# Kernel optimization log

Hardware: AMD Instinct MI355X
Metric: run time of the kernel (lower is better)

The kernel has to match this reference:

```python
import jax, jax.numpy as jnp
import numpy as np

N = 100000
E = 1600000
NODE_DIM = 64
H = 128
NUM_LAYERS = 3
NUM_CLASSES = 6
NUM_GRAPHS = 512
LN_EPS = 1e-5


def setup_inputs() -> dict:
    key = jax.random.key(0)
    ks = jax.random.split(key, 16)
    s = 0.05
    x = jax.random.normal(ks[0], (N, NODE_DIM), jnp.float32)
    edge_index = jax.random.randint(ks[1], (2, E), 0, N, dtype=jnp.int64)
    batch = jnp.sort(jax.random.randint(ks[2], (N,), 0, NUM_GRAPHS, dtype=jnp.int64))
    return {
        "x": x,
        "edge_index": edge_index,
        "batch": batch,
        "proj_w": jax.random.normal(ks[3], (NODE_DIM, H), jnp.float32) * s,
        "proj_b": jnp.zeros((H,), jnp.float32),
        "lin_l_w": jax.random.normal(ks[4], (NUM_LAYERS, H, H), jnp.float32) * s,
        "lin_l_b": jnp.zeros((NUM_LAYERS, H), jnp.float32),
        "lin_r_w": jax.random.normal(ks[5], (NUM_LAYERS, H, H), jnp.float32) * s,
        "ln_g": jnp.ones((NUM_LAYERS, H), jnp.float32),
        "ln_b": jnp.zeros((NUM_LAYERS, H), jnp.float32),
        "gate_w1": jax.random.normal(ks[6], (H, H // 2), jnp.float32) * s,
        "gate_b1": jnp.zeros((H // 2,), jnp.float32),
        "gate_w2": jax.random.normal(ks[7], (H // 2, 1), jnp.float32) * s,
        "gate_b2": jnp.zeros((1,), jnp.float32),
        "cls_w1": jax.random.normal(ks[8], (H, H // 2), jnp.float32) * s,
        "cls_b1": jnp.zeros((H // 2,), jnp.float32),
        "cls_w2": jax.random.normal(ks[9], (H // 2, NUM_CLASSES), jnp.float32) * s,
        "cls_b2": jnp.zeros((NUM_CLASSES,), jnp.float32),
    }


def _layer_norm(x, g, b):
    mu = jnp.mean(x, axis=-1, keepdims=True)
    var = jnp.mean(jnp.square(x - mu), axis=-1, keepdims=True)
    return (x - mu) * jax.lax.rsqrt(var + LN_EPS) * g + b


def _sage_mean_aggr(x, src, dst):
    # mean of source node features grouped by destination node
    summed = jax.ops.segment_sum(x[src], dst, num_segments=N)  # [N,H]
    deg = jax.ops.segment_sum(jnp.ones((E,), x.dtype), dst, num_segments=N)
    return summed / jnp.maximum(deg, 1.0)[:, None]


def reference(x, edge_index, batch, proj_w, proj_b, lin_l_w, lin_l_b, lin_r_w,
              ln_g, ln_b, gate_w1, gate_b1, gate_w2, gate_b2,
              cls_w1, cls_b1, cls_w2, cls_b2):
    src, dst = edge_index[0], edge_index[1]
    h = jax.nn.relu(x @ proj_w + proj_b)  # [N,H]
    for l in range(NUM_LAYERS):
        r = h
        aggr = _sage_mean_aggr(h, src, dst)
        # PyG SAGEConv: lin_l(aggregated) + lin_r(self), bias only in lin_l
        h = aggr @ lin_l_w[l] + lin_l_b[l] + h @ lin_r_w[l]
        h = _layer_norm(h, ln_g[l], ln_b[l])
        h = jax.nn.elu(h)
        h = h + r  # dropout is identity in eval mode
    # GlobalAttention pooling: segment softmax over nodes per graph
    gate = (jax.nn.relu(h @ gate_w1 + gate_b1) @ gate_w2 + gate_b2)[:, 0]  # [N]
    gmax = jax.ops.segment_max(gate, batch, num_segments=NUM_GRAPHS)
    eg = jnp.exp(gate - gmax[batch])
    denom = jax.ops.segment_sum(eg, batch, num_segments=NUM_GRAPHS)
    alpha = eg / denom[batch]  # [N]
    pooled = jax.ops.segment_sum(h * alpha[:, None], batch, num_segments=NUM_GRAPHS)  # [G,H]
    out = jax.nn.relu(pooled @ cls_w1 + cls_b1) @ cls_w2 + cls_b2  # [G,C]
    return out
```

## Files before the change

### kernel.cpp

```cpp
#include <hip/hip_runtime.h>
#include <hip/hip_fp16.h>
#include <math.h>

#define N_NODES   100000
#define N_EDGES   1600000
#define NDIM      64
#define H         128
#define NUM_LAYERS 3
#define NUM_CLASSES 6
#define NUM_GRAPHS 512
#define LN_EPS    1e-5f
#define NBKT      391
#define SCAP      5376
#define BPAD      136

typedef _Float16 f16x8 __attribute__((ext_vector_type(8)));
typedef float    f32x4 __attribute__((ext_vector_type(4)));

__device__ __forceinline__ int idx_at(const int* raw, int is64, int i) {
    return is64 ? raw[2 * (long long)i] : raw[i];
}
__device__ __forceinline__ int lower_bound(const int* a, int n, int v) {
    int lo = 0, hi = n;
    while (lo < hi) { int m = (lo + hi) >> 1; if (a[m] < v) lo = m + 1; else hi = m; }
    return lo;
}

__device__ __forceinline__ f32x4 gload16(const __half* __restrict__ base, int voff) {
    f32x4 r;
    asm volatile("global_load_dwordx4 %0, %1, %2"
                 : "=v"(r) : "v"(voff), "s"(base));
    return r;
}

__global__ void k_detect(const int* eraw, const int* braw, int* flags,
                         int* bcnt, float* gate_z) {
    int i = blockIdx.x * blockDim.x + threadIdx.x;
    if (i < 512) bcnt[i] = 0;
    if (i < 64) gate_z[i] = 0.f;
    if (i == 0) {
        int e64 = 1;
        for (int k = 1; k < 128; k += 2) if (eraw[k] != 0) { e64 = 0; break; }
        flags[0] = e64;
        flags[1] = (braw[N_NODES - 1] == 0) ? 1 : 0;
    }
}

__global__ void k_conv_batch(const int* braw, const int* flags, int* batch32) {
    int i = blockIdx.x * blockDim.x + threadIdx.x;
    if (i < N_NODES) batch32[i] = idx_at(braw, flags[1], i);
}

__global__ __launch_bounds__(256) void k_bhist(const int* eraw, const int* flags, int* bcnt) {
    __shared__ int c[512];
    int tid = threadIdx.x;
    for (int i = tid; i < 512; i += 256) c[i] = 0;
    __syncthreads();
    int f = flags[0];
    int stride = gridDim.x * 256;
    for (int e = blockIdx.x * 256 + tid; e < N_EDGES; e += stride) {
        int d = idx_at(eraw, f, N_EDGES + e);
        atomicAdd(&c[d >> 8], 1);
    }
    __syncthreads();
    for (int i = tid; i < 512; i += 256) if (c[i]) atomicAdd(&bcnt[i], c[i]);
}

__global__ void k_bscan(const int* bcnt, int* boff, int* bcursor) {
    __shared__ int sh[512];
    int tid = threadIdx.x;
    int v = bcnt[tid];
    sh[tid] = v;
    __syncthreads();
    for (int off = 1; off < 512; off <<= 1) {
        int u = (tid >= off) ? sh[tid - off] : 0;
        __syncthreads();
        sh[tid] += u;
        __syncthreads();
    }
    int excl = sh[tid] - v;
    boff[tid] = excl;
    bcursor[tid] = excl;
    if (tid == 511) boff[512] = sh[511];
}

#define EPB 4096
__global__ __launch_bounds__(256) void k_bucket(const int* eraw, const int* flags,
                                                int* bcursor, unsigned int* br) {
    __shared__ int cnt[512];
    __shared__ int excl[512];
    __shared__ int resv[512];
    __shared__ int lcur[512];
    __shared__ int psum[256];
    __shared__ unsigned int srec[EPB];
    __shared__ unsigned short sbkt[EPB];
    int tid = threadIdx.x;
    int f = flags[0];
    int base = blockIdx.x * EPB;
    int se[16], de[16];
#pragma unroll
    for (int j = 0; j < 16; ++j) {
        int e = base + j * 256 + tid;
        if (e < N_EDGES) {
            se[j] = idx_at(eraw, f, e);
            de[j] = idx_at(eraw, f, N_EDGES + e);
        } else de[j] = -1;
    }
    for (int i = tid; i < 512; i += 256) cnt[i] = 0;
    __syncthreads();
#pragma unroll
    for (int j = 0; j < 16; ++j)
        if (de[j] >= 0) atomicAdd(&cnt[de[j] >> 8], 1);
    __syncthreads();
    int b0 = cnt[2 * tid], b1 = cnt[2 * tid + 1];
    psum[tid] = b0 + b1;
    __syncthreads();
    for (int off = 1; off < 256; off <<= 1) {
        int u = (tid >= off) ? psum[tid - off] : 0;
        __syncthreads();
        psum[tid] += u;
        __syncthreads();
    }
    int pex = psum[tid] - (b0 + b1);
    excl[2 * tid] = pex;
    excl[2 * tid + 1] = pex + b0;
    lcur[2 * tid] = pex;
    lcur[2 * tid + 1] = pex + b0;
    resv[2 * tid]     = b0 ? atomicAdd(&bcursor[2 * tid], b0) : 0;
    resv[2 * tid + 1] = b1 ? atomicAdd(&bcursor[2 * tid + 1], b1) : 0;
    __syncthreads();
#pragma unroll
    for (int j = 0; j < 16; ++j)
        if (de[j] >= 0) {
            int b = de[j] >> 8;
            int slot = atomicAdd(&lcur[b], 1);
            srec[slot] = ((unsigned int)(de[j] & 255) << 24) | (unsigned int)se[j];
            sbkt[slot] = (unsigned short)b;
        }
    __syncthreads();
    int vtot = psum[255];
    for (int s2 = tid; s2 < vtot; s2 += 256) {
        int b = sbkt[s2];
        br[resv[b] + (s2 - excl[b])] = srec[s2];
    }
}

__global__ __launch_bounds__(256) void k_csr_tail(const unsigned int* br, const int* boff,
                                                  int* rowptr, int* col) {
    __shared__ int d256[256];
    __shared__ int sc[256];
    __shared__ int cbuf[SCAP];
    int b = blockIdx.x;
    int tid = threadIdx.x;
    int lo = boff[b], hi = boff[b + 1];
    int wsize = hi - lo;
    d256[tid] = 0;
    __syncthreads();
    for (int i = lo + tid; i < hi; i += 256)
        atomicAdd(&d256[br[i] >> 24], 1);
    __syncthreads();
    int v = d256[tid];
    sc[tid] = v;
    __syncthreads();
    for (int off = 1; off < 256; off <<= 1) {
        int u = (tid >= off) ? sc[tid - off] : 0;
        __syncthreads();
        sc[tid] += u;
        __syncthreads();
    }
    int excl = sc[tid] - v;
    int node = (b << 8) + tid;
    if (node < N_NODES) rowptr[node] = lo + excl;
    if (b == NBKT - 1 && tid == 0) rowptr[N_NODES] = N_EDGES;
    __syncthreads();
    d256[tid] = excl;
    __syncthreads();
    if (wsize <= SCAP) {
        for (int i = lo + tid; i < hi; i += 256) {
            unsigned int r = br[i];
            int p = atomicAdd(&d256[r >> 24], 1);
            cbuf[p] = (int)(r & 0xFFFFFF);
        }
        __syncthreads();
        for (int j = tid; j < wsize; j += 256) col[lo + j] = cbuf[j] << 8;
    } else {
        for (int i = lo + tid; i < hi; i += 256) {
            unsigned int r = br[i];
            int p = atomicAdd(&d256[r >> 24], 1);
            col[lo + p] = (int)(r & 0xFFFFFF) << 8;
        }
    }
}

__global__ void k_prepw(const float* __restrict__ lin_l_w, const float* __restrict__ lin_r_w,
                        const float* __restrict__ gate_w1,
                        __half* __restrict__ W16t, __half* __restrict__ W16g) {
    int i = blockIdx.x * 256 + threadIdx.x;
    if (i < NUM_LAYERS * 128 * 256) {
        int l = i >> 15;
        int rem = i & 32767;
        int n = rem >> 8;
        int k = rem & 255;
        float v = (k < 128) ? lin_l_w[(size_t)l * 16384 + k * 128 + n]
                            : lin_r_w[(size_t)l * 16384 + (k - 128) * 128 + n];
        W16t[(size_t)l * 32768 + n * 256 + k] = __float2half(v);
    } else if (i < NUM_LAYERS * 128 * 256 + 64 * 128) {
        int idx = i - NUM_LAYERS * 128 * 256;
        int n = idx >> 7;
        int k = idx & 127;
        W16g[n * 128 + k] = __float2half(gate_w1[k * 64 + n]);
    }
}

__global__ __launch_bounds__(256) void k_gemm_proj(const float* __restrict__ A,
                                                   const float* __restrict__ W,
                                                   const float* __restrict__ bias,
                                                   __half* __restrict__ C16,
                                                   int nrows, int K) {
    __shared__ float As_t[32][68];
    __shared__ float Ws[32 * 128];
    int tid = threadIdx.x;
    int row0 = blockIdx.x * 64;
    int tr = tid >> 4;
    int tc = tid & 15;
    int c0 = tc * 8;
    float acc[4][8];
#pragma unroll
    for (int i = 0; i < 4; ++i)
#pragma unroll
        for (int j = 0; j < 8; ++j) acc[i][j] = 0.f;

    for (int kc = 0; kc < K; kc += 32) {
        __syncthreads();
#pragma unroll
        for (int it = 0; it < 2; ++it) {
            int idx = tid + it * 256;
            int r = idx >> 3, c4 = idx & 7;
            int gr = row0 + r;
            float4 v = make_float4(0.f, 0.f, 0.f, 0.f);
            if (gr < nrows) v = *(const float4*)(A + (size_t)gr * K + kc + c4 * 4);
            As_t[c4 * 4 + 0][r] = v.x;
            As_t[c4 * 4 + 1][r] = v.y;
            As_t[c4 * 4 + 2][r] = v.z;
            As_t[c4 * 4 + 3][r] = v.w;
        }
#pragma unroll
        for (int it = 0; it < 4; ++it) {
            int idx = tid + it * 256;
            int r = idx >> 5, c4 = idx & 31;
            *(float4*)(&Ws[r * 128 + c4 * 4]) = *(const float4*)(W + (size_t)(kc + r) * 128 + c4 * 4);
        }
        __syncthreads();
#pragma unroll
        for (int k = 0; k < 32; ++k) {
            float4 a4 = *(const float4*)(&As_t[k][tr * 4]);
            float a[4] = {a4.x, a4.y, a4.z, a4.w};
            float4 w0 = *(const float4*)(&Ws[k * 128 + c0]);
            float4 w1 = *(const float4*)(&Ws[k * 128 + c0 + 4]);
            float w[8] = {w0.x, w0.y, w0.z, w0.w, w1.x, w1.y, w1.z, w1.w};
#pragma unroll
            for (int i = 0; i < 4; ++i)
#pragma unroll
                for (int j = 0; j < 8; ++j) acc[i][j] += a[i] * w[j];
        }
    }
    float bv[8];
#pragma unroll
    for (int j = 0; j < 8; ++j) bv[j] = bias[c0 + j];
#pragma unroll
    for (int i = 0; i < 4; ++i) {
        int gr = row0 + tr * 4 + i;
        if (gr < nrows) {
            float o[8];
#pragma unroll
            for (int j = 0; j < 8; ++j) o[j] = fmaxf(acc[i][j] + bv[j], 0.f);
            __half2 p[4];
#pragma unroll
            for (int j = 0; j < 8; j += 2) p[j / 2] = __floats2half2_rn(o[j], o[j + 1]);
            *(float4*)(C16 + (size_t)gr * 128 + c0) = *(float4*)p;
        }
    }
}

__global__ __launch_bounds__(256) void k_gate_mfma(const __half* __restrict__ h16,
                                                   const __half* __restrict__ W16g,
                                                   const float* __restrict__ b1,
                                                   const float* __restrict__ w2,
                                                   const float* __restrict__ b2,
                                                   float* __restrict__ gate) {
    __shared__ __half Bs[64 * BPAD];
    int tid = threadIdx.x;
    int wave = tid >> 6, lane = tid & 63;
    int s = lane & 15, quad = lane >> 4;
    int row0 = blockIdx.x * 64 + wave * 16;
    int arow = row0 + s;
    if (arow >= N_NODES) arow = N_NODES - 1;

#pragma unroll
    for (int it = 0; it < 4; ++it) {
        int idx = tid + it * 256;
        int n = idx >> 4, ch = idx & 15;
        *(float4*)(&Bs[n * BPAD + ch * 8]) = *(const float4*)(W16g + (size_t)n * 128 + ch * 8);
    }
    __syncthreads();

    f32x4 acc[4];
#pragma unroll
    for (int c = 0; c < 4; ++c) acc[c] = (f32x4){0.f, 0.f, 0.f, 0.f};

    const __half* aptr = h16 + (size_t)arow * H;
#pragma unroll
    for (int kc = 0; kc < 128; kc += 32) {
        f16x8 afrag = *(const f16x8*)(aptr + kc + quad * 8);
#pragma unroll
        for (int c = 0; c < 4; ++c) {
            f16x8 bfrag = *(const f16x8*)(&Bs[(c * 16 + s) * BPAD + kc + quad * 8]);
            acc[c] = __builtin_amdgcn_mfma_f32_16x16x32_f16(afrag, bfrag, acc[c], 0, 0, 0);
        }
    }
    float part[4] = {0.f, 0.f, 0.f, 0.f};
#pragma unroll
    for (int c = 0; c < 4; ++c) {
        float bv = b1[c * 16 + s];
        float wv = w2[c * 16 + s];
#pragma unroll
        for (int i = 0; i < 4; ++i)
            part[i] += fmaxf(acc[c][i] + bv, 0.f) * wv;
    }
#pragma unroll
    for (int off = 1; off < 16; off <<= 1) {
#pragma unroll
        for (int i = 0; i < 4; ++i) part[i] += __shfl_xor(part[i], off);
    }
    if (s == 0) {
        float b2v = b2[0];
#pragma unroll
        for (int i = 0; i < 4; ++i) {
            int r = row0 + quad * 4 + i;
            if (r < N_NODES) gate[r] = part[i] + b2v;
        }
    }
}

__global__ __launch_bounds__(64) void k_softmax_g(float* __restrict__ gate,
                                                  const int* __restrict__ batch32,
                                                  float* __restrict__ gsum) {
    int g = blockIdx.x;
    int lane = threadIdx.x;
    int n0 = lower_bound(batch32, N_NODES, g);
    int n1 = lower_bound(batch32, N_NODES, g + 1);
    float m = -INFINITY;
    for (int n = n0 + lane; n < n1; n += 64) m = fmaxf(m, gate[n]);
#pragma unroll
    for (int off = 32; off >= 1; off >>= 1) m = fmaxf(m, __shfl_xor(m, off));
    float s = 0.f;
    for (int n = n0 + lane; n < n1; n += 64) {
        float e = expf(gate[n] - m);
        gate[n] = e;
        s += e;
    }
#pragma unroll
    for (int off = 32; off >= 1; off >>= 1) s += __shfl_xor(s, off);
    if (lane == 0) gsum[g] = s;
}

__global__ __launch_bounds__(256) void k_pool_g(const __half* __restrict__ h16,
                                                const float* __restrict__ eg,
                                                const float* __restrict__ gsum,
                                                const int* __restrict__ batch32,
                                                float* __restrict__ pooled) {
    __shared__ float sx[256], sy[256];
    int g = blockIdx.x;
    int tid = threadIdx.x;
    int c2 = tid & 63;
    int p = tid >> 6;
    int n0 = lower_bound(batch32, N_NODES, g);
    int n1 = lower_bound(batch32, N_NODES, g + 1);
    float ax = 0.f, ay = 0.f;
    for (int n = n0 + p; n < n1; n += 4) {
        __half2 v = *(const __half2*)(h16 + (size_t)n * H + c2 * 2);
        float2 fv = __half22float2(v);
        float w = eg[n];
        ax += w * fv.x;
        ay += w * fv.y;
    }
    sx[tid] = ax; sy[tid] = ay;
    __syncthreads();
    if (tid < 64) {
        float s = gsum[g];
        float vx = sx[tid] + sx[tid + 64] + sx[tid + 128] + sx[tid + 192];
        float vy = sy[tid] + sy[tid + 64] + sy[tid + 128] + sy[tid + 192];
        float2 o;
        o.x = (n1 > n0) ? vx / s : 0.f;
        o.y = (n1 > n0) ? vy / s : 0.f;
        *(float2*)(pooled + (size_t)g * H + c2 * 2) = o;
    }
}

__global__ __launch_bounds__(256) void k_layer_mfma(const __half* __restrict__ t16,
                                                    __half* __restrict__ h16,
                                                    const __half* __restrict__ W16t,
                                                    const float* __restrict__ bl,
                                                    const float* __restrict__ g,
                                                    const float* __restrict__ bb) {
    __shared__ __half Bs[128 * BPAD];
    int tid = threadIdx.x;
    int wave = tid >> 6, lane = tid & 63;
    int s = lane & 15, quad = lane >> 4;
    int row0 = blockIdx.x * 64;
    int wrow0 = row0 + wave * 16;
    int arow = wrow0 + s;
    if (arow >= N_NODES) arow = N_NODES - 1;

    f32x4 acc[8];
#pragma unroll
    for (int c = 0; c < 8; ++c) acc[c] = (f32x4){0.f, 0.f, 0.f, 0.f};

#pragma unroll
    for (int ph = 0; ph < 2; ++ph) {
        __syncthreads();
#pragma unroll
        for (int it = 0; it < 8; ++it) {
            int idx = tid + it * 256;
            int n = idx >> 4, ch = idx & 15;
            *(float4*)(&Bs[n * BPAD + ch * 8]) =
                *(const float4*)(W16t + (size_t)n * 256 + ph * 128 + ch * 8);
        }
        __syncthreads();
        const __half* aptr = (ph ? h16 : t16) + (size_t)arow * H;
#pragma unroll
        for (int kk = 0; kk < 128; kk += 32) {
            f16x8 afrag = *(const f16x8*)(aptr + kk + quad * 8);
#pragma unroll
            for (int c = 0; c < 8; ++c) {
                f16x8 bfrag = *(const f16x8*)(&Bs[(c * 16 + s) * BPAD + kk + quad * 8]);
                acc[c] = __builtin_amdgcn_mfma_f32_16x16x32_f16(afrag, bfrag, acc[c], 0, 0, 0);
            }
        }
    }

    float y[8][4];
    float sm[4] = {0.f, 0.f, 0.f, 0.f}, sq[4] = {0.f, 0.f, 0.f, 0.f};
#pragma unroll
    for (int c = 0; c < 8; ++c) {
        float bv = bl[c * 16 + s];
#pragma unroll
        for (int i = 0; i < 4; ++i) {
            float v = acc[c][i] + bv;
            y[c][i] = v;
            sm[i] += v;
            sq[i] += v * v;
        }
    }
#pragma unroll
    for (int off = 1; off < 16; off <<= 1) {
#pragma unroll
        for (int i = 0; i < 4; ++i) {
            sm[i] += __shfl_xor(sm[i], off);
            sq[i] += __shfl_xor(sq[i], off);
        }
    }
    float mean[4], rstd[4];
#pragma unroll
    for (int i = 0; i < 4; ++i) {
        mean[i] = sm[i] * (1.0f / H);
        float var = sq[i] * (1.0f / H) - mean[i] * mean[i];
        rstd[i] = rsqrtf(var + LN_EPS);
    }
    float gv[8], bbv[8];
#pragma unroll
    for (int c = 0; c < 8; ++c) { gv[c] = g[c * 16 + s]; bbv[c] = bb[c * 16 + s]; }

    __syncthreads();
#pragma unroll
    for (int i = 0; i < 4; ++i) {
        int lr = wave * 16 + quad * 4 + i;
#pragma unroll
        for (int c = 0; c < 8; ++c) {
            float yv = (y[c][i] - mean[i]) * rstd[i] * gv[c] + bbv[c];
            yv = yv > 0.f ? yv : expf(yv) - 1.f;
            Bs[lr * BPAD + c * 16 + s] = __float2half(yv);
        }
    }
    __syncthreads();
#pragma unroll
    for (int it = 0; it < 4; ++it) {
        int idx = tid + it * 256;
        int r = idx >> 4, ch = idx & 15;
        int grow = row0 + r;
        if (grow < N_NODES) {
            float4 sv = *(float4*)(&Bs[r * BPAD + ch * 8]);
            float4 hv = *(const float4*)(h16 + (size_t)grow * H + ch * 8);
            __half2* pa = (__half2*)&sv;
            const __half2* pb = (const __half2*)&hv;
#pragma unroll
            for (int j = 0; j < 4; ++j) {
                float2 fa = __half22float2(pa[j]);
                float2 fb = __half22float2(pb[j]);
                pa[j] = __floats2half2_rn(fa.x + fb.x, fa.y + fb.y);
            }
            *(float4*)(h16 + (size_t)grow * H + ch * 8) = sv;
        }
    }
}

__global__ __launch_bounds__(256) void k_aggr(const __half* __restrict__ h16,
                                              const int* __restrict__ rowptr,
                                              const int* __restrict__ col,
                                              __half* __restrict__ t16,
                                              int zoff) {
    int lane = threadIdx.x & 63;
    int node = blockIdx.x * 4 + (threadIdx.x >> 6);
    if (node >= N_NODES) return;
    int s = lane & 15;
    int g = lane >> 4;
    int soff = s * 16;
    int e0 = rowptr[node];
    int deg = rowptr[node + 1] - e0;

    if (deg == 0) {
        if (g == 0) {
            float4 zz = make_float4(0.f, 0.f, 0.f, 0.f);
            *(float4*)(t16 + (size_t)node * H + s * 8) = zz;
        }
        return;
    }

    __half2 z = __floats2half2_rn(0.f, 0.f);
    __half2 ac[4][4];
#pragma unroll
    for (int a = 0; a < 4; ++a)
#pragma unroll
        for (int k = 0; k < 4; ++k) ac[a][k] = z;

    {
        int cb[8];
#pragma unroll
        for (int j = 0; j < 8; ++j) {
            int ei = g + 4 * j;
            cb[j] = col[e0 + (ei < deg ? ei : 0)];
        }
#pragma unroll
        for (int j = 0; j < 8; ++j) {
            int ei = g + 4 * j;
            cb[j] = ((ei < deg) ? cb[j] : zoff) + soff;
        }
        __builtin_amdgcn_sched_barrier(0);
        f32x4 rv[8];
#pragma unroll
        for (int j = 0; j < 8; ++j) rv[j] = gload16(h16, cb[j]);
        asm volatile("s_waitcnt vmcnt(0)" ::: "memory");
        __builtin_amdgcn_sched_barrier(0);
#pragma unroll
        for (int j = 0; j < 8; ++j) {
            const __half2* hv = (const __half2*)&rv[j];
            int a = j & 3;
            ac[a][0] = __hadd2(ac[a][0], hv[0]);
            ac[a][1] = __hadd2(ac[a][1], hv[1]);
            ac[a][2] = __hadd2(ac[a][2], hv[2]);
            ac[a][3] = __hadd2(ac[a][3], hv[3]);
        }
    }

    if (deg > 32) {
        for (int base = 32; base < deg; base += 32) {
            int cb[8];
#pragma unroll
            for (int j = 0; j < 8; ++j) {
                int ei = base + g + 4 * j;
                cb[j] = col[e0 + (ei < deg ? ei : base)];
            }
#pragma unroll
            for (int j = 0; j < 8; ++j) {
                int ei = base + g + 4 * j;
                cb[j] = ((ei < deg) ? cb[j] : zoff) + soff;
            }
            __builtin_amdgcn_sched_barrier(0);
            f32x4 rv[8];
#pragma unroll
            for (int j = 0; j < 8; ++j) rv[j] = gload16(h16, cb[j]);
            asm volatile("s_waitcnt vmcnt(0)" ::: "memory");
            __builtin_amdgcn_sched_barrier(0);
#pragma unroll
            for (int j = 0; j < 8; ++j) {
                const __half2* hv = (const __half2*)&rv[j];
                int a = j & 3;
                ac[a][0] = __hadd2(ac[a][0], hv[0]);
                ac[a][1] = __hadd2(ac[a][1], hv[1]);
                ac[a][2] = __hadd2(ac[a][2], hv[2]);
                ac[a][3] = __hadd2(ac[a][3], hv[3]);
            }
        }
    }

    float f[8];
#pragma unroll
    for (int k = 0; k < 4; ++k) {
        float2 s0 = __half22float2(ac[0][k]);
        float2 s1 = __half22float2(ac[1][k]);
        float2 s2 = __half22float2(ac[2][k]);
        float2 s3 = __half22float2(ac[3][k]);
        f[2 * k]     = (s0.x + s1.x) + (s2.x + s3.x);
        f[2 * k + 1] = (s0.y + s1.y) + (s2.y + s3.y);
    }
#pragma unroll
    for (int off = 16; off <= 32; off <<= 1) {
#pragma unroll
        for (int k = 0; k < 8; ++k) f[k] += __shfl_xor(f[k], off);
    }
    if (g == 0) {
        float inv = 1.0f / (float)(deg > 1 ? deg : 1);
        __half2 o[4];
#pragma unroll
        for (int k = 0; k < 4; ++k)
            o[k] = __floats2half2_rn(f[2 * k] * inv, f[2 * k + 1] * inv);
        *(float4*)(t16 + (size_t)node * H + s * 8) = *(float4*)o;
    }
}

__global__ __launch_bounds__(64) void k_cls(const float* __restrict__ pooled,
                                            const float* __restrict__ w1,
                                            const float* __restrict__ b1,
                                            const float* __restrict__ w2,
                                            const float* __restrict__ b2,
                                            float* __restrict__ out) {
    __shared__ float sp[64];
    int g = blockIdx.x;
    int lane = threadIdx.x;
    float r0 = pooled[(size_t)g * H + lane];
    float r1 = pooled[(size_t)g * H + 64 + lane];
    float acc = b1[lane];
#pragma unroll 16
    for (int k = 0; k < 64; ++k) acc += __shfl(r0, k) * w1[k * 64 + lane];
#pragma unroll 16
    for (int k = 0; k < 64; ++k) acc += __shfl(r1, k) * w1[(64 + k) * 64 + lane];
    sp[lane] = fmaxf(acc, 0.f);
    __syncthreads();
    if (lane < NUM_CLASSES) {
        float o = b2[lane];
        for (int c = 0; c < 64; ++c) o += sp[c] * w2[c * NUM_CLASSES + lane];
        out[g * NUM_CLASSES + lane] = o;
    }
}

extern "C" void kernel_launch(void* const* d_in, const int* in_sizes, int n_in,
                              void* d_out, int out_size, void* d_ws, size_t ws_size,
                              hipStream_t stream) {
    const float* x       = (const float*)d_in[0];
    const int*   eraw    = (const int*)d_in[1];
    const int*   braw    = (const int*)d_in[2];
    const float* proj_w  = (const float*)d_in[3];
    const float* proj_b  = (const float*)d_in[4];
    const float* lin_l_w = (const float*)d_in[5];
    const float* lin_l_b = (const float*)d_in[6];
    const float* lin_r_w = (const float*)d_in[7];
    const float* ln_g    = (const float*)d_in[8];
    const float* ln_b    = (const float*)d_in[9];
    const float* gate_w1 = (const float*)d_in[10];
    const float* gate_b1 = (const float*)d_in[11];
    const float* gate_w2 = (const float*)d_in[12];
    const float* gate_b2 = (const float*)d_in[13];
    const float* cls_w1  = (const float*)d_in[14];
    const float* cls_b1  = (const float*)d_in[15];
    const float* cls_w2  = (const float*)d_in[16];
    const float* cls_b2  = (const float*)d_in[17];
    float* out = (float*)d_out;

    __half* h16    = (__half*)d_ws;
    __half* t16    = h16 + (size_t)N_NODES * H;
    float*  gate   = (float*)(t16 + (size_t)N_NODES * H);
    float*  gsum   = gate + N_NODES;
    float*  pooled = gsum + NUM_GRAPHS;
    __half* W16t   = (__half*)(pooled + NUM_GRAPHS * H);
    __half* W16g   = W16t + (size_t)NUM_LAYERS * 32768;
    int* flags     = (int*)(W16g + 64 * 128);
    int* col       = flags + 4;
    int* batch32   = col + N_EDGES;
    int* rowptr    = batch32 + N_NODES;
    int* bcnt      = rowptr + N_NODES + 1;
    int* boff      = bcnt + 512;
    int* bcursor   = boff + 513;
    unsigned int* br = (unsigned int*)(bcursor + 512);

    const int zoff = (int)((const char*)gate - (const char*)h16);

    const int nbN = (N_NODES + 255) / 256;
    const int nbE4 = (N_EDGES + EPB - 1) / EPB;
    const int nbW = (N_NODES + 3) / 4;
    const int nbG = (N_NODES + 63) / 64;
    const int nbP = (NUM_LAYERS * 128 * 256 + 64 * 128 + 255) / 256;

    k_detect<<<2, 256, 0, stream>>>(eraw, braw, flags, bcnt, gate);
    k_conv_batch<<<nbN, 256, 0, stream>>>(braw, flags, batch32);
    k_bhist<<<512, 256, 0, stream>>>(eraw, flags, bcnt);
    k_bscan<<<1, 512, 0, stream>>>(bcnt, boff, bcursor);
    k_bucket<<<nbE4, 256, 0, stream>>>(eraw, flags, bcursor, br);
    k_csr_tail<<<NBKT, 256, 0, stream>>>(br, boff, rowptr, col);
    k_prepw<<<nbP, 256, 0, stream>>>(lin_l_w, lin_r_w, gate_w1, W16t, W16g);

    k_gemm_proj<<<nbG, 256, 0, stream>>>(x, proj_w, proj_b, h16, N_NODES, NDIM);

    for (int l = 0; l < NUM_LAYERS; ++l) {
        const float* bl  = lin_l_b + (size_t)l * H;
        const float* gl  = ln_g + (size_t)l * H;
        const float* blb = ln_b + (size_t)l * H;
        k_aggr<<<nbW, 256, 0, stream>>>(h16, rowptr, col, t16, zoff);
        k_layer_mfma<<<nbG, 256, 0, stream>>>(t16, h16, W16t + (size_t)l * 32768, bl, gl, blb);
    }

    k_gate_mfma<<<nbG, 256, 0, stream>>>(h16, W16g, gate_b1, gate_w2, gate_b2, gate);
    k_softmax_g<<<NUM_GRAPHS, 64, 0, stream>>>(gate, batch32, gsum);
    k_pool_g<<<NUM_GRAPHS, 256, 0, stream>>>(h16, gate, gsum, batch32, pooled);
    k_cls<<<NUM_GRAPHS, 64, 0, stream>>>(pooled, cls_w1, cls_b1, cls_w2, cls_b2, out);
}
```

Measured before the change: 475.5 us.

## Store node features in column-sliced planar layout and slice aggregation by feature block

Node features move from row-major [N,128] fp16 to 8 planar slices of 16 halves per node, so each slice of the feature matrix (3.2MB) can stay resident in cache during the gather. The aggregation kernel now assigns each block a fixed slice (blockIdx & 7) and loops over nodes, with 16 lanes gathering 8-byte chunks per edge and reducing through shuffles. All GEMM, residual, gate and pool kernels are updated to address the new layout. The trade-off is smaller 8-byte loads, more total passes over rowptr/col (once per slice), and less memory-level parallelism per wave.

```diff
diff --git a/kernel.cpp b/kernel.cpp
--- a/kernel.cpp
+++ b/kernel.cpp
@@ -13,6 +13,7 @@
 #define NBKT      391
 #define SCAP      5376
 #define BPAD      136
+#define PLH32     (N_NODES * 16)
 
 typedef _Float16 f16x8 __attribute__((ext_vector_type(8)));
 typedef float    f32x4 __attribute__((ext_vector_type(4)));
@@ -25,10 +26,13 @@
     while (lo < hi) { int m = (lo + hi) >> 1; if (a[m] < v) lo = m + 1; else hi = m; }
     return lo;
 }
-
-__device__ __forceinline__ f32x4 gload16(const __half* __restrict__ base, int voff) {
-    f32x4 r;
-    asm volatile("global_load_dwordx4 %0, %1, %2"
+__device__ __forceinline__ size_t pmoff(int c, int n) {
+    return (size_t)(c >> 1) * PLH32 + (size_t)n * 16 + (size_t)((c & 1) * 8);
+}
+
+__device__ __forceinline__ float2 gload8(const __half* __restrict__ base, int voff) {
+    float2 r;
+    asm volatile("global_load_dwordx2 %0, %1, %2"
                  : "=v"(r) : "v"(voff), "s"(base));
     return r;
 }
@@ -182,12 +186,12 @@
             cbuf[p] = (int)(r & 0xFFFFFF);
         }
         __syncthreads();
-        for (int j = tid; j < wsize; j += 256) col[lo + j] = cbuf[j] << 8;
+        for (int j = tid; j < wsize; j += 256) col[lo + j] = cbuf[j] << 5;
     } else {
         for (int i = lo + tid; i < hi; i += 256) {
             unsigned int r = br[i];
             int p = atomicAdd(&d256[r >> 24], 1);
-            col[lo + p] = (int)(r & 0xFFFFFF) << 8;
+            col[lo + p] = (int)(r & 0xFFFFFF) << 5;
         }
     }
 }
@@ -277,7 +281,7 @@
             __half2 p[4];
 #pragma unroll
             for (int j = 0; j < 8; j += 2) p[j / 2] = __floats2half2_rn(o[j], o[j + 1]);
-            *(float4*)(C16 + (size_t)gr * 128 + c0) = *(float4*)p;
+            *(float4*)(C16 + pmoff(tc, gr)) = *(float4*)p;
         }
     }
 }
@@ -308,10 +312,9 @@
 #pragma unroll
     for (int c = 0; c < 4; ++c) acc[c] = (f32x4){0.f, 0.f, 0.f, 0.f};
 
-    const __half* aptr = h16 + (size_t)arow * H;
 #pragma unroll
     for (int kc = 0; kc < 128; kc += 32) {
-        f16x8 afrag = *(const f16x8*)(aptr + kc + quad * 8);
+        f16x8 afrag = *(const f16x8*)(h16 + pmoff(kc / 8 + quad, arow));
 #pragma unroll
         for (int c = 0; c < 4; ++c) {
             f16x8 bfrag = *(const f16x8*)(&Bs[(c * 16 + s) * BPAD + kc + quad * 8]);
@@ -378,7 +381,7 @@
     int n1 = lower_bound(batch32, N_NODES, g + 1);
     float ax = 0.f, ay = 0.f;
     for (int n = n0 + p; n < n1; n += 4) {
-        __half2 v = *(const __half2*)(h16 + (size_t)n * H + c2 * 2);
+        __half2 v = *(const __half2*)(h16 + pmoff(c2 >> 2, n) + (c2 & 3) * 2);
         float2 fv = __half22float2(v);
         float w = eg[n];
         ax += w * fv.x;
@@ -427,10 +430,10 @@
                 *(const float4*)(W16t + (size_t)n * 256 + ph * 128 + ch * 8);
         }
         __syncthreads();
-        const __half* aptr = (ph ? h16 : t16) + (size_t)arow * H;
+        const __half* aptr = ph ? h16 : t16;
 #pragma unroll
         for (int kk = 0; kk < 128; kk += 32) {
-            f16x8 afrag = *(const f16x8*)(aptr + kk + quad * 8);
+            f16x8 afrag = *(const f16x8*)(aptr + pmoff(kk / 8 + quad, arow));
 #pragma unroll
             for (int c = 0; c < 8; ++c) {
                 f16x8 bfrag = *(const f16x8*)(&Bs[(c * 16 + s) * BPAD + kk + quad * 8]);
@@ -486,11 +489,11 @@
 #pragma unroll
     for (int it = 0; it < 4; ++it) {
         int idx = tid + it * 256;
-        int r = idx >> 4, ch = idx & 15;
+        int r = idx & 63, ch = idx >> 6;
         int grow = row0 + r;
         if (grow < N_NODES) {
             float4 sv = *(float4*)(&Bs[r * BPAD + ch * 8]);
-            float4 hv = *(const float4*)(h16 + (size_t)grow * H + ch * 8);
+            float4 hv = *(const float4*)(h16 + pmoff(ch, grow));
             __half2* pa = (__half2*)&sv;
             const __half2* pb = (const __half2*)&hv;
 #pragma unroll
@@ -499,7 +502,7 @@
                 float2 fb = __half22float2(pb[j]);
                 pa[j] = __floats2half2_rn(fa.x + fb.x, fa.y + fb.y);
             }
-            *(float4*)(h16 + (size_t)grow * H + ch * 8) = sv;
+            *(float4*)(h16 + pmoff(ch, grow)) = sv;
         }
     }
 }
@@ -509,112 +512,62 @@
                                               const int* __restrict__ col,
                                               __half* __restrict__ t16,
                                               int zoff) {
-    int lane = threadIdx.x & 63;
-    int node = blockIdx.x * 4 + (threadIdx.x >> 6);
-    if (node >= N_NODES) return;
-    int s = lane & 15;
-    int g = lane >> 4;
-    int soff = s * 16;
-    int e0 = rowptr[node];
-    int deg = rowptr[node + 1] - e0;
-
-    if (deg == 0) {
-        if (g == 0) {
-            float4 zz = make_float4(0.f, 0.f, 0.f, 0.f);
-            *(float4*)(t16 + (size_t)node * H + s * 8) = zz;
-        }
-        return;
-    }
-
-    __half2 z = __floats2half2_rn(0.f, 0.f);
-    __half2 ac[4][4];
-#pragma unroll
-    for (int a = 0; a < 4; ++a)
-#pragma unroll
-        for (int k = 0; k < 4; ++k) ac[a][k] = z;
-
-    {
-        int cb[8];
-#pragma unroll
-        for (int j = 0; j < 8; ++j) {
-            int ei = g + 4 * j;
-            cb[j] = col[e0 + (ei < deg ? ei : 0)];
-        }
-#pragma unroll
-        for (int j = 0; j < 8; ++j) {
-            int ei = g + 4 * j;
-            cb[j] = ((ei < deg) ? cb[j] : zoff) + soff;
-        }
+    int tid = threadIdx.x;
+    int lane = tid & 63;
+    int slice = blockIdx.x & 7;
+    int wv = (blockIdx.x >> 3) * 4 + (tid >> 6);
+    int e = lane >> 2;
+    int q = lane & 3;
+    int pboff = slice * (N_NODES * 32);
+    int qb = q * 8;
+
+    for (int node = wv; node < N_NODES; node += 12500) {
+        int e0 = rowptr[node];
+        int deg = rowptr[node + 1] - e0;
+        int i1 = 16 + e;
+        int c0 = col[e0 + (e < deg ? e : 0)];
+        int c1 = col[e0 + (i1 < deg ? i1 : 0)];
+        int v0 = (e < deg) ? (pboff + c0 + qb) : zoff;
+        int v1 = (i1 < deg) ? (pboff + c1 + qb) : zoff;
         __builtin_amdgcn_sched_barrier(0);
-        f32x4 rv[8];
-#pragma unroll
-        for (int j = 0; j < 8; ++j) rv[j] = gload16(h16, cb[j]);
+        float2 r0 = gload8(h16, v0);
+        float2 r1 = gload8(h16, v1);
         asm volatile("s_waitcnt vmcnt(0)" ::: "memory");
         __builtin_amdgcn_sched_barrier(0);
-#pragma unroll
-        for (int j = 0; j < 8; ++j) {
-            const __half2* hv = (const __half2*)&rv[j];
-            int a = j & 3;
-            ac[a][0] = __hadd2(ac[a][0], hv[0]);
-            ac[a][1] = __hadd2(ac[a][1], hv[1]);
-            ac[a][2] = __hadd2(ac[a][2], hv[2]);
-            ac[a][3] = __hadd2(ac[a][3], hv[3]);
-        }
-    }
-
-    if (deg > 32) {
-        for (int base = 32; base < deg; base += 32) {
-            int cb[8];
-#pragma unroll
-            for (int j = 0; j < 8; ++j) {
-                int ei = base + g + 4 * j;
-                cb[j] = col[e0 + (ei < deg ? ei : base)];
+        const __half2* h0 = (const __half2*)&r0;
+        const __half2* h1 = (const __half2*)&r1;
+        __half2 a0 = __hadd2(h0[0], h1[0]);
+        __half2 a1 = __hadd2(h0[1], h1[1]);
+
+        if (deg > 32) {
+            for (int base = 32; base < deg; base += 16) {
+                int ii = base + e;
+                int cc = col[e0 + (ii < deg ? ii : base)];
+                int vv = (ii < deg) ? (pboff + cc + qb) : zoff;
+                float2 rr = gload8(h16, vv);
+                asm volatile("s_waitcnt vmcnt(0)" ::: "memory");
+                const __half2* hh = (const __half2*)&rr;
+                a0 = __hadd2(a0, hh[0]);
+                a1 = __hadd2(a1, hh[1]);
             }
-#pragma unroll
-            for (int j = 0; j < 8; ++j) {
-                int ei = base + g + 4 * j;
-                cb[j] = ((ei < deg) ? cb[j] : zoff) + soff;
-            }
-            __builtin_amdgcn_sched_barrier(0);
-            f32x4 rv[8];
-#pragma unroll
-            for (int j = 0; j < 8; ++j) rv[j] = gload16(h16, cb[j]);
-            asm volatile("s_waitcnt vmcnt(0)" ::: "memory");
-            __builtin_amdgcn_sched_barrier(0);
-#pragma unroll
-            for (int j = 0; j < 8; ++j) {
-                const __half2* hv = (const __half2*)&rv[j];
-                int a = j & 3;
-                ac[a][0] = __hadd2(ac[a][0], hv[0]);
-                ac[a][1] = __hadd2(ac[a][1], hv[1]);
-                ac[a][2] = __hadd2(ac[a][2], hv[2]);
-                ac[a][3] = __hadd2(ac[a][3], hv[3]);
-            }
-        }
-    }
-
-    float f[8];
-#pragma unroll
-    for (int k = 0; k < 4; ++k) {
-        float2 s0 = __half22float2(ac[0][k]);
-        float2 s1 = __half22float2(ac[1][k]);
-        float2 s2 = __half22float2(ac[2][k]);
-        float2 s3 = __half22float2(ac[3][k]);
-        f[2 * k]     = (s0.x + s1.x) + (s2.x + s3.x);
-        f[2 * k + 1] = (s0.y + s1.y) + (s2.y + s3.y);
-    }
-#pragma unroll
-    for (int off = 16; off <= 32; off <<= 1) {
-#pragma unroll
-        for (int k = 0; k < 8; ++k) f[k] += __shfl_xor(f[k], off);
-    }
-    if (g == 0) {
-        float inv = 1.0f / (float)(deg > 1 ? deg : 1);
-        __half2 o[4];
-#pragma unroll
-        for (int k = 0; k < 4; ++k)
-            o[k] = __floats2half2_rn(f[2 * k] * inv, f[2 * k + 1] * inv);
-        *(float4*)(t16 + (size_t)node * H + s * 8) = *(float4*)o;
+        }
+
+#pragma unroll
+        for (int off = 4; off <= 32; off <<= 1) {
+            int t0 = __shfl_xor(*(int*)&a0, off);
+            int t1 = __shfl_xor(*(int*)&a1, off);
+            a0 = __hadd2(a0, *(__half2*)&t0);
+            a1 = __hadd2(a1, *(__half2*)&t1);
+        }
+        if (e == 0) {
+            float2 f0 = __half22float2(a0);
+            float2 f1 = __half22float2(a1);
+            float inv = 1.0f / (float)(deg > 1 ? deg : 1);
+            float2 ov;
+            ((__half2*)&ov)[0] = __floats2half2_rn(f0.x * inv, f0.y * inv);
+            ((__half2*)&ov)[1] = __floats2half2_rn(f1.x * inv, f1.y * inv);
+            *(float2*)((char*)t16 + pboff + node * 32 + qb) = ov;
+        }
     }
 }
 
@@ -686,7 +639,7 @@
 
     const int nbN = (N_NODES + 255) / 256;
     const int nbE4 = (N_EDGES + EPB - 1) / EPB;
-    const int nbW = (N_NODES + 3) / 4;
+    const int nbA = 25000;
     const int nbG = (N_NODES + 63) / 64;
     const int nbP = (NUM_LAYERS * 128 * 256 + 64 * 128 + 255) / 256;
 
@@ -704,7 +657,7 @@
         const float* bl  = lin_l_b + (size_t)l * H;
         const float* gl  = ln_g + (size_t)l * H;
         const float* blb = ln_b + (size_t)l * H;
-        k_aggr<<<nbW, 256, 0, stream>>>(h16, rowptr, col, t16, zoff);
+        k_aggr<<<nbA, 256, 0, stream>>>(h16, rowptr, col, t16, zoff);
         k_layer_mfma<<<nbG, 256, 0, stream>>>(t16, h16, W16t + (size_t)l * 32768, bl, gl, blb);
     }
 
```

Measured after the change: 704.6 us. 48.2% more time.
